# Kernel optimization log

Hardware: AMD Instinct MI355X
Metric: run time of the kernel (lower is better)

The kernel has to match this reference:

```python
import jax, jax.numpy as jnp
import numpy as np

B, S, E, H, FF = 8, 1024, 1024, 16, 4096
DK = E // H
EPS = 1.1920929e-07  # torch RMSNorm default eps = finfo(float32).eps


def _rmsnorm(x, g):
    return x * jax.lax.rsqrt(jnp.mean(x * x, axis=-1, keepdims=True) + EPS) * g


def _rope(q, k):
    # q, k: [B, H, S, DK]; standard rotate-half RoPE, theta=10000
    d = q.shape[-1]
    s = q.shape[-2]
    inv_freq = 1.0 / (10000.0 ** (jnp.arange(0, d, 2, dtype=jnp.float32) / d))
    ang = jnp.arange(s, dtype=jnp.float32)[:, None] * inv_freq  # [S, d/2]
    cos = jnp.concatenate([jnp.cos(ang), jnp.cos(ang)], axis=-1)  # [S, d]
    sin = jnp.concatenate([jnp.sin(ang), jnp.sin(ang)], axis=-1)

    def rot(x):
        x1, x2 = jnp.split(x, 2, axis=-1)
        return jnp.concatenate([-x2, x1], axis=-1)

    return q * cos + rot(q) * sin, k * cos + rot(k) * sin


def setup_inputs() -> dict:
    key = jax.random.key(0)
    ks = jax.random.split(key, 16)
    sc = 0.02
    inp = {
        "x": jax.random.normal(ks[0], (B, S, E), dtype=jnp.float32),
        "WQ": jax.random.normal(ks[1], (E, E), dtype=jnp.float32) * sc,
        "bQ": jnp.zeros((E,), jnp.float32),
        "WK": jax.random.normal(ks[2], (E, E), dtype=jnp.float32) * sc,
        "bK": jnp.zeros((E,), jnp.float32),
        "WV": jax.random.normal(ks[3], (E, E), dtype=jnp.float32) * sc,
        "bV": jnp.zeros((E,), jnp.float32),
        "WO": jax.random.normal(ks[4], (E, E), dtype=jnp.float32) * sc,
        "bO": jnp.zeros((E,), jnp.float32),
        "W1": jax.random.normal(ks[5], (E, FF), dtype=jnp.float32) * sc,
        "b1": jnp.zeros((FF,), jnp.float32),
        "W2": jax.random.normal(ks[6], (FF, E), dtype=jnp.float32) * sc,
        "b2": jnp.zeros((E,), jnp.float32),
        "g1": jnp.ones((E,), jnp.float32),
        "g2": jnp.ones((E,), jnp.float32),
    }
    return inp


def reference(x, WQ, bQ, WK, bK, WV, bV, WO, bO, W1, b1, W2, b2, g1, g2):
    b, s, e = x.shape

    def attn(h):
        q = (h @ WQ + bQ).reshape(b, s, H, DK).transpose(0, 2, 1, 3)
        k = (h @ WK + bK).reshape(b, s, H, DK).transpose(0, 2, 1, 3)
        v = (h @ WV + bV).reshape(b, s, H, DK).transpose(0, 2, 1, 3)
        q, k = _rope(q, k)
        scores = jnp.einsum("bhqd,bhkd->bhqk", q, k) / jnp.sqrt(jnp.float32(DK))
        p = jax.nn.softmax(scores, axis=-1)
        o = jnp.einsum("bhqk,bhkd->bhqd", p, v)
        o = o.transpose(0, 2, 1, 3).reshape(b, s, e)
        return o @ WO + bO

    def ffn(h):
        return jax.nn.relu(h @ W1 + b1) @ W2 + b2

    x = x + attn(_rmsnorm(x, g1))
    x = x + ffn(_rmsnorm(x, g2))
    return x
```

## Files before the change

### kernel.cpp

```cpp
#include <hip/hip_runtime.h>
#include <math.h>

#define B_ 8
#define S_ 1024
#define E_ 1024
#define H_ 16
#define FF_ 4096

typedef __attribute__((ext_vector_type(8))) short bf16x8;
typedef __attribute__((ext_vector_type(4))) float f32x4;

#define QSCALE 0.1803368801111f
#define LG2_10K 0.4152410118f

__device__ __forceinline__ unsigned short f2bf(float f) {
  union { float f; unsigned u; } v;
  v.f = f;
  unsigned r = v.u + 0x7fffu + ((v.u >> 16) & 1u);
  return (unsigned short)(r >> 16);
}
__device__ __forceinline__ float bf2f(unsigned short u) {
  union { unsigned u; float f; } v;
  v.u = ((unsigned)u) << 16;
  return v.f;
}
__device__ __forceinline__ unsigned fbits(float f) {
  union { float f; unsigned u; } v;
  v.f = f;
  return v.u;
}

__device__ __forceinline__ void glds16(const void* g, void* l) {
  __builtin_amdgcn_global_load_lds(
      (const __attribute__((address_space(1))) unsigned int*)g,
      (__attribute__((address_space(3))) unsigned int*)l, 16, 0, 0);
}

__global__ __launch_bounds__(256) void prep(const float* __restrict__ WQ,
                                            const float* __restrict__ WK,
                                            const float* __restrict__ WV,
                                            const float* __restrict__ WO,
                                            const float* __restrict__ W1,
                                            const float* __restrict__ W2,
                                            const float* __restrict__ bQ,
                                            const float* __restrict__ bK,
                                            const float* __restrict__ bV,
                                            unsigned short* __restrict__ WQKVt,
                                            unsigned short* __restrict__ WOt,
                                            unsigned short* __restrict__ W1t,
                                            unsigned short* __restrict__ W2t,
                                            float* __restrict__ bqkv) {
  const int id = blockIdx.x;
  if (id >= 12288) {
    const int i = (id - 12288) * 256 + threadIdx.x;
    if (i < 3072)
      bqkv[i] = (i < 1024) ? bQ[i] : ((i < 2048) ? bK[i - 1024] : bV[i - 2048]);
    return;
  }
  const float* W;
  unsigned short* D;
  int K, N, x, y;
  if (id < 4096) {
    const int m = id >> 10;
    const float* ws4[4] = {WQ, WK, WV, WO};
    unsigned short* ds4[4] = {WQKVt, WQKVt + 1024 * 1024, WQKVt + 2 * 1024 * 1024, WOt};
    W = ws4[m]; D = ds4[m]; K = 1024; N = 1024;
    x = id & 31; y = (id >> 5) & 31;
  } else if (id < 8192) {
    const int j = id - 4096;
    W = W1; D = W1t; K = 1024; N = 4096;
    x = j & 127; y = j >> 7;
  } else {
    const int j = id - 8192;
    W = W2; D = W2t; K = 4096; N = 1024;
    x = j & 31; y = j >> 5;
  }
  __shared__ float t[32][33];
  const int tx = threadIdx.x & 31, ty = threadIdx.x >> 5;
  const int n0 = x * 32, k0 = y * 32;
#pragma unroll
  for (int p = 0; p < 4; ++p)
    t[ty + p * 8][tx] = W[(size_t)(k0 + ty + p * 8) * N + n0 + tx];
  __syncthreads();
#pragma unroll
  for (int p = 0; p < 4; ++p)
    D[(size_t)(n0 + ty + p * 8) * K + k0 + tx] = f2bf(t[tx][ty + p * 8]);
}

__global__ __launch_bounds__(256) void rmsnorm_kernel(const float* __restrict__ x,
                                                      const float* __restrict__ g,
                                                      unsigned short* __restrict__ out) {
  const int row = blockIdx.x;
  const int t = threadIdx.x;
  const float4 v = ((const float4*)(x + (size_t)row * E_))[t];
  float ss = v.x * v.x + v.y * v.y + v.z * v.z + v.w * v.w;
#pragma unroll
  for (int off = 32; off > 0; off >>= 1) ss += __shfl_down(ss, off);
  __shared__ float sred[4];
  if ((t & 63) == 0) sred[t >> 6] = ss;
  __syncthreads();
  const float tot = sred[0] + sred[1] + sred[2] + sred[3];
  const float rinv = rsqrtf(tot * (1.0f / E_) + 1.1920929e-07f);
  const float4 gv = ((const float4*)g)[t];
  ushort4 o;
  o.x = f2bf(v.x * rinv * gv.x);
  o.y = f2bf(v.y * rinv * gv.y);
  o.z = f2bf(v.z * rinv * gv.z);
  o.w = f2bf(v.w * rinv * gv.w);
  ((ushort4*)(out + (size_t)row * E_))[t] = o;
}


template <int OUT_BF16, int RELU, int RES>
__global__ __launch_bounds__(256) void gemm_bf16(const unsigned short* __restrict__ A,
                                                 const unsigned short* __restrict__ Bt,
                                                 const float* __restrict__ bias,
                                                 const float* __restrict__ res,
                                                 void* __restrict__ C,
                                                 int M, int N, int K) {
  __shared__ unsigned short As[128 * 64];
  __shared__ unsigned short Bs[128 * 64];
  const int tid = threadIdx.x;
  const int w = tid >> 6;
  const int lane = tid & 63;

  const int nb = gridDim.x;
  const int id = blockIdx.x;
  const int lid = (id & 7) * (nb >> 3) + (id >> 3);
  const int per = (M >> 7) * 8;
  const int grp = lid / per;
  const int rem = lid - grp * per;
  const int bn = (grp * 8 + (rem & 7)) * 128;
  const int bm = (rem >> 3) * 128;

  const int wm = (w & 1) * 64, wn = (w >> 1) * 64;

  f32x4 acc[4][4];
#pragma unroll
  for (int i = 0; i < 4; ++i)
#pragma unroll
    for (int j = 0; j < 4; ++j) acc[i][j] = (f32x4){0.f, 0.f, 0.f, 0.f};

  const int srow = lane >> 3;
  const int skb = (lane & 7) ^ srow;
  const unsigned short* Ap[4];
  const unsigned short* Bp[4];
  unsigned short* AsD[4];
  unsigned short* BsD[4];
#pragma unroll
  for (int p = 0; p < 4; ++p) {
    const int u = w * 4 + p;
    Ap[p] = A + (size_t)(bm + u * 8 + srow) * K + skb * 8;
    Bp[p] = Bt + (size_t)(bn + u * 8 + srow) * K + skb * 8;
    AsD[p] = &As[u * 512 + lane * 8];
    BsD[p] = &Bs[u * 512 + lane * 8];
  }

  const int fr = lane & 15;
  const int g = lane >> 4;
  const int sw = fr & 7;

  for (int k0 = 0; k0 < K; k0 += 64) {
    __syncthreads();
#pragma unroll
    for (int p = 0; p < 4; ++p) glds16(Ap[p] + k0, AsD[p]);
#pragma unroll
    for (int p = 0; p < 4; ++p) glds16(Bp[p] + k0, BsD[p]);
    __syncthreads();
    bf16x8 a[4][2], b[4][2];
#pragma unroll
    for (int im = 0; im < 4; ++im)
#pragma unroll
      for (int kc = 0; kc < 2; ++kc)
        a[im][kc] = *(const bf16x8*)&As[(wm + im * 16 + fr) * 64 + ((kc * 4 + g) ^ sw) * 8];
#pragma unroll
    for (int in = 0; in < 4; ++in)
#pragma unroll
      for (int kc = 0; kc < 2; ++kc)
        b[in][kc] = *(const bf16x8*)&Bs[(wn + in * 16 + fr) * 64 + ((kc * 4 + g) ^ sw) * 8];
#pragma unroll
    for (int im = 0; im < 4; ++im)
#pragma unroll
      for (int in = 0; in < 4; ++in) {
        acc[im][in] = __builtin_amdgcn_mfma_f32_16x16x32_bf16(a[im][0], b[in][0], acc[im][in], 0, 0, 0);
        acc[im][in] = __builtin_amdgcn_mfma_f32_16x16x32_bf16(a[im][1], b[in][1], acc[im][in], 0, 0, 0);
      }
  }

#pragma unroll
  for (int im = 0; im < 4; ++im) {
    const int row0 = bm + wm + im * 16 + (lane >> 4) * 4;
#pragma unroll
    for (int in = 0; in < 4; ++in) {
      const int col = bn + wn + in * 16 + fr;
      const float bv = bias[col];
#pragma unroll
      for (int r = 0; r < 4; ++r) {
        float v = acc[im][in][r] + bv;
        if (RES) v += res[(size_t)(row0 + r) * N + col];
        if (RELU) v = fmaxf(v, 0.0f);
        if (OUT_BF16)
          ((unsigned short*)C)[(size_t)(row0 + r) * N + col] = f2bf(v);
        else
          ((float*)C)[(size_t)(row0 + r) * N + col] = v;
      }
    }
  }
}

__global__ __launch_bounds__(256) void gemm_sk2(const unsigned short* __restrict__ A,
                                                const unsigned short* __restrict__ Bt,
                                                unsigned short* __restrict__ Pp) {
  const int N = 1024, K = 4096, KH = 2048;
  __shared__ unsigned short As[128 * 64];
  __shared__ unsigned short Bs[128 * 64];
  const int tid = threadIdx.x;
  const int w = tid >> 6;
  const int lane = tid & 63;

  const int id = blockIdx.x;
  const int kh = id >> 9;
  const int hid = id & 511;
  const int lid = (hid & 7) * 64 + (hid >> 3);
  const int bn = (lid & 7) * 128;
  const int bm = (lid >> 3) * 128;

  const int wm = (w & 1) * 64, wn = (w >> 1) * 64;

  f32x4 acc[4][4];
#pragma unroll
  for (int i = 0; i < 4; ++i)
#pragma unroll
    for (int j = 0; j < 4; ++j) acc[i][j] = (f32x4){0.f, 0.f, 0.f, 0.f};

  const int srow = lane >> 3;
  const int skb = (lane & 7) ^ srow;
  const unsigned short* Ap[4];
  const unsigned short* Bp[4];
  unsigned short* AsD[4];
  unsigned short* BsD[4];
#pragma unroll
  for (int p = 0; p < 4; ++p) {
    const int u = w * 4 + p;
    Ap[p] = A + (size_t)(bm + u * 8 + srow) * K + kh * KH + skb * 8;
    Bp[p] = Bt + (size_t)(bn + u * 8 + srow) * K + kh * KH + skb * 8;
    AsD[p] = &As[u * 512 + lane * 8];
    BsD[p] = &Bs[u * 512 + lane * 8];
  }

  const int fr = lane & 15;
  const int g = lane >> 4;
  const int sw = fr & 7;

  for (int k0 = 0; k0 < KH; k0 += 64) {
    __syncthreads();
#pragma unroll
    for (int p = 0; p < 4; ++p) glds16(Ap[p] + k0, AsD[p]);
#pragma unroll
    for (int p = 0; p < 4; ++p) glds16(Bp[p] + k0, BsD[p]);
    __syncthreads();
    bf16x8 a[4][2], b[4][2];
#pragma unroll
    for (int im = 0; im < 4; ++im)
#pragma unroll
      for (int kc = 0; kc < 2; ++kc)
        a[im][kc] = *(const bf16x8*)&As[(wm + im * 16 + fr) * 64 + ((kc * 4 + g) ^ sw) * 8];
#pragma unroll
    for (int in = 0; in < 4; ++in)
#pragma unroll
      for (int kc = 0; kc < 2; ++kc)
        b[in][kc] = *(const bf16x8*)&Bs[(wn + in * 16 + fr) * 64 + ((kc * 4 + g) ^ sw) * 8];
#pragma unroll
    for (int im = 0; im < 4; ++im)
#pragma unroll
      for (int in = 0; in < 4; ++in) {
        acc[im][in] = __builtin_amdgcn_mfma_f32_16x16x32_bf16(a[im][0], b[in][0], acc[im][in], 0, 0, 0);
        acc[im][in] = __builtin_amdgcn_mfma_f32_16x16x32_bf16(a[im][1], b[in][1], acc[im][in], 0, 0, 0);
      }
  }

  unsigned short* P = Pp + (size_t)kh * (8u << 20);
#pragma unroll
  for (int im = 0; im < 4; ++im) {
    const int row0 = bm + wm + im * 16 + (lane >> 4) * 4;
#pragma unroll
    for (int in = 0; in < 4; ++in) {
      const int col = bn + wn + in * 16 + fr;
#pragma unroll
      for (int r = 0; r < 4; ++r)
        P[(size_t)(row0 + r) * N + col] = f2bf(acc[im][in][r]);
    }
  }
}

__global__ __launch_bounds__(256) void ff2_reduce(const unsigned short* __restrict__ Pp,
                                                  const float* __restrict__ x1,
                                                  const float* __restrict__ b2,
                                                  float* __restrict__ out) {
  const int i = blockIdx.x * 256 + threadIdx.x;
  const size_t off = (size_t)i * 4;
  const ushort4 p0 = *(const ushort4*)(Pp + off);
  const ushort4 p1 = *(const ushort4*)(Pp + (8u << 20) + off);
  const float4 xv = *(const float4*)(x1 + off);
  const float4 bv = *(const float4*)(b2 + (off & 1023));
  float4 o;
  o.x = xv.x + bv.x + bf2f(p0.x) + bf2f(p1.x);
  o.y = xv.y + bv.y + bf2f(p0.y) + bf2f(p1.y);
  o.z = xv.z + bv.z + bf2f(p0.z) + bf2f(p1.z);
  o.w = xv.w + bv.w + bf2f(p0.w) + bf2f(p1.w);
  *(float4*)(out + off) = o;
}

template <int OUT_BF16, int RELU, int RES>
__global__ __launch_bounds__(256) void gemm_n64(const unsigned short* __restrict__ A,
                                                const unsigned short* __restrict__ Bt,
                                                const float* __restrict__ bias,
                                                const float* __restrict__ res,
                                                void* __restrict__ C,
                                                int M, int N, int K) {
  __shared__ unsigned short As[128 * 64];
  __shared__ unsigned short Bs[64 * 64];
  const int tid = threadIdx.x;
  const int w = tid >> 6;
  const int lane = tid & 63;

  const int nbn = N >> 6;
  const int bm = (blockIdx.x / nbn) * 128;
  const int bn = (blockIdx.x % nbn) * 64;

  const int wm = (w & 1) * 64, wn = (w >> 1) * 32;

  f32x4 acc[4][2];
#pragma unroll
  for (int i = 0; i < 4; ++i)
#pragma unroll
    for (int j = 0; j < 2; ++j) acc[i][j] = (f32x4){0.f, 0.f, 0.f, 0.f};

  const int srow = lane >> 3;
  const int skb = (lane & 7) ^ srow;
  const unsigned short* Ap[4];
  const unsigned short* Bp[2];
  unsigned short* AsD[4];
  unsigned short* BsD[2];
#pragma unroll
  for (int p = 0; p < 4; ++p) {
    const int u = w * 4 + p;
    Ap[p] = A + (size_t)(bm + u * 8 + srow) * K + skb * 8;
    AsD[p] = &As[u * 512 + lane * 8];
  }
#pragma unroll
  for (int p = 0; p < 2; ++p) {
    const int u = w * 2 + p;
    Bp[p] = Bt + (size_t)(bn + u * 8 + srow) * K + skb * 8;
    BsD[p] = &Bs[u * 512 + lane * 8];
  }

  const int fr = lane & 15;
  const int g = lane >> 4;
  const int sw = fr & 7;

  for (int k0 = 0; k0 < K; k0 += 64) {
    __syncthreads();
#pragma unroll
    for (int p = 0; p < 4; ++p) glds16(Ap[p] + k0, AsD[p]);
#pragma unroll
    for (int p = 0; p < 2; ++p) glds16(Bp[p] + k0, BsD[p]);
    __syncthreads();
    bf16x8 a[4][2], b[2][2];
#pragma unroll
    for (int im = 0; im < 4; ++im)
#pragma unroll
      for (int kc = 0; kc < 2; ++kc)
        a[im][kc] = *(const bf16x8*)&As[(wm + im * 16 + fr) * 64 + ((kc * 4 + g) ^ sw) * 8];
#pragma unroll
    for (int in = 0; in < 2; ++in)
#pragma unroll
      for (int kc = 0; kc < 2; ++kc)
        b[in][kc] = *(const bf16x8*)&Bs[(wn + in * 16 + fr) * 64 + ((kc * 4 + g) ^ sw) * 8];
#pragma unroll
    for (int im = 0; im < 4; ++im)
#pragma unroll
      for (int in = 0; in < 2; ++in) {
        acc[im][in] = __builtin_amdgcn_mfma_f32_16x16x32_bf16(a[im][0], b[in][0], acc[im][in], 0, 0, 0);
        acc[im][in] = __builtin_amdgcn_mfma_f32_16x16x32_bf16(a[im][1], b[in][1], acc[im][in], 0, 0, 0);
      }
  }

#pragma unroll
  for (int im = 0; im < 4; ++im) {
    const int row0 = bm + wm + im * 16 + (lane >> 4) * 4;
#pragma unroll
    for (int in = 0; in < 2; ++in) {
      const int col = bn + wn + in * 16 + fr;
      const float bv = bias[col];
#pragma unroll
      for (int r = 0; r < 4; ++r) {
        float v = acc[im][in][r] + bv;
        if (RES) v += res[(size_t)(row0 + r) * N + col];
        if (RELU) v = fmaxf(v, 0.0f);
        if (OUT_BF16)
          ((unsigned short*)C)[(size_t)(row0 + r) * N + col] = f2bf(v);
        else
          ((float*)C)[(size_t)(row0 + r) * N + col] = v;
      }
    }
  }
}

__global__ __launch_bounds__(256) void gemm_qkv(const unsigned short* __restrict__ A,
                                                const unsigned short* __restrict__ Bt,
                                                const float* __restrict__ bias,
                                                unsigned short* __restrict__ QKV,
                                                unsigned short* __restrict__ Vt,
                                                int M, int K) {
  __shared__ unsigned short As[128 * 64];
  __shared__ unsigned short Bs[128 * 64];
  const int tid = threadIdx.x;
  const int w = tid >> 6;
  const int lane = tid & 63;

  const int nb = gridDim.x;
  const int id = blockIdx.x;
  const int lid = (id & 7) * (nb >> 3) + (id >> 3);
  const int per = (M >> 7) * 8;
  const int grp = lid / per;
  const int rem = lid - grp * per;
  const int bn = (grp * 8 + (rem & 7)) * 128;
  const int bm = (rem >> 3) * 128;

  const int wm = (w & 1) * 64, wn = (w >> 1) * 64;

  f32x4 acc[4][4];
#pragma unroll
  for (int i = 0; i < 4; ++i)
#pragma unroll
    for (int j = 0; j < 4; ++j) acc[i][j] = (f32x4){0.f, 0.f, 0.f, 0.f};

  const int srow = lane >> 3;
  const int skb = (lane & 7) ^ srow;
  const unsigned short* Ap[4];
  const unsigned short* Bp[4];
  unsigned short* AsD[4];
  unsigned short* BsD[4];
#pragma unroll
  for (int p = 0; p < 4; ++p) {
    const int u = w * 4 + p;
    Ap[p] = A + (size_t)(bm + u * 8 + srow) * K + skb * 8;
    Bp[p] = Bt + (size_t)(bn + u * 8 + srow) * K + skb * 8;
    AsD[p] = &As[u * 512 + lane * 8];
    BsD[p] = &Bs[u * 512 + lane * 8];
  }

  const int fr = lane & 15;
  const int g = lane >> 4;
  const int sw = fr & 7;

  for (int k0 = 0; k0 < K; k0 += 64) {
    __syncthreads();
#pragma unroll
    for (int p = 0; p < 4; ++p) glds16(Ap[p] + k0, AsD[p]);
#pragma unroll
    for (int p = 0; p < 4; ++p) glds16(Bp[p] + k0, BsD[p]);
    __syncthreads();
    bf16x8 a[4][2], b[4][2];
#pragma unroll
    for (int im = 0; im < 4; ++im)
#pragma unroll
      for (int kc = 0; kc < 2; ++kc)
        a[im][kc] = *(const bf16x8*)&As[(wm + im * 16 + fr) * 64 + ((kc * 4 + g) ^ sw) * 8];
#pragma unroll
    for (int in = 0; in < 4; ++in)
#pragma unroll
      for (int kc = 0; kc < 2; ++kc)
        b[in][kc] = *(const bf16x8*)&Bs[(wn + in * 16 + fr) * 64 + ((kc * 4 + g) ^ sw) * 8];
#pragma unroll
    for (int im = 0; im < 4; ++im)
#pragma unroll
      for (int in = 0; in < 4; ++in) {
        acc[im][in] = __builtin_amdgcn_mfma_f32_16x16x32_bf16(a[im][0], b[in][0], acc[im][in], 0, 0, 0);
        acc[im][in] = __builtin_amdgcn_mfma_f32_16x16x32_bf16(a[im][1], b[in][1], acc[im][in], 0, 0, 0);
      }
  }

  const int cbase = bn + wn;
  const int seg = cbase >> 6;
  const int typ = seg >> 4;
  const int hh = seg & 15;
  const int bidx = bm >> 10;
  float bv[4];
#pragma unroll
  for (int in = 0; in < 4; ++in) bv[in] = bias[cbase + in * 16 + fr];

  if (typ == 2) {
#pragma unroll
    for (int im = 0; im < 4; ++im) {
      const int s0 = (bm & 1023) + wm + im * 16 + (lane >> 4) * 4;
#pragma unroll
      for (int in = 0; in < 4; ++in) {
        const int d = in * 16 + fr;
        ushort4 o4;
        o4.x = f2bf(acc[im][in][0] + bv[in]);
        o4.y = f2bf(acc[im][in][1] + bv[in]);
        o4.z = f2bf(acc[im][in][2] + bv[in]);
        o4.w = f2bf(acc[im][in][3] + bv[in]);
        *(ushort4*)&Vt[(size_t)((bidx * 16 + hh) * 64 + d) * S_ + s0] = o4;
      }
    }
  } else {
    const float qs = (typ == 0) ? QSCALE : 1.0f;
    const float i0 = exp2f(-LG2_10K * (float)fr);
    const float i1 = exp2f(-LG2_10K * (float)(fr + 16));
#pragma unroll
    for (int im = 0; im < 4; ++im) {
      const int row0 = bm + wm + im * 16 + (lane >> 4) * 4;
#pragma unroll
      for (int r = 0; r < 4; ++r) {
        const int row = row0 + r;
        const float s = (float)(row & 1023);
        float sn0, cs0, sn1, cs1;
        __sincosf(s * i0, &sn0, &cs0);
        __sincosf(s * i1, &sn1, &cs1);
        const float x0 = acc[im][0][r] + bv[0];
        const float x1 = acc[im][1][r] + bv[1];
        const float x2 = acc[im][2][r] + bv[2];
        const float x3 = acc[im][3][r] + bv[3];
        unsigned short* cp = QKV + (size_t)row * 3072 + cbase;
        cp[fr]      = f2bf((x0 * cs0 - x2 * sn0) * qs);
        cp[16 + fr] = f2bf((x1 * cs1 - x3 * sn1) * qs);
        cp[32 + fr] = f2bf((x2 * cs0 + x0 * sn0) * qs);
        cp[48 + fr] = f2bf((x3 * cs1 + x1 * sn1) * qs);
      }
    }
  }
}

__global__ __launch_bounds__(256) void attn_v4(const unsigned short* __restrict__ QKV,
                                               const unsigned short* __restrict__ Vt,
                                               unsigned short* __restrict__ Og) {
  __shared__ unsigned short Kf[2][8 * 512];
  __shared__ unsigned short Vf[2][8 * 512];
  __shared__ unsigned short Ps[4][32 * 72];
  const int tid = threadIdx.x;
  const int w = tid >> 6, lane = tid & 63;
  const int qt = blockIdx.x, bh = blockIdx.y;
  const int b = bh >> 4, h = bh & 15;
  const int fr = lane & 15, g = lane >> 4, fk = g * 8;
  const int q0w = qt * 128 + w * 32;

  bf16x8 qB[2][2];
#pragma unroll
  for (int nt = 0; nt < 2; ++nt)
#pragma unroll
    for (int c = 0; c < 2; ++c)
      qB[nt][c] = *(const bf16x8*)&QKV[(size_t)(b * S_ + q0w + nt * 16 + fr) * 3072 +
                                       h * 64 + c * 32 + fk];

  f32x4 o[4][2];
#pragma unroll
  for (int mt = 0; mt < 4; ++mt)
#pragma unroll
    for (int nt = 0; nt < 2; ++nt) o[mt][nt] = (f32x4){0.f, 0.f, 0.f, 0.f};
  float l[2] = {0.0f, 0.0f};

#define STAGE(kt, bufi)                                                                   \
  {                                                                                       \
    _Pragma("unroll") for (int p = 0; p < 4; ++p) {                                       \
      const int u = w * 4 + p;                                                            \
      if (u < 8) {                                                                        \
        const int mt = u >> 1, c = u & 1;                                                 \
        glds16(QKV + (size_t)(b * S_ + (kt) * 64 + mt * 16 + fr) * 3072 + 1024 + h * 64 + \
                   c * 32 + fk,                                                           \
               &Kf[bufi][u * 512]);                                                       \
      } else {                                                                            \
        const int v2 = u - 8, mt = v2 >> 1, c = v2 & 1;                                   \
        glds16(Vt + (size_t)(bh * 64 + mt * 16 + fr) * S_ + (kt) * 64 + c * 32 + fk,      \
               &Vf[bufi][v2 * 512]);                                                      \
      }                                                                                   \
    }                                                                                     \
  }

  STAGE(0, 0);

  for (int kt = 0; kt < 16; ++kt) {
    __syncthreads();
    if (kt < 15) STAGE(kt + 1, (kt + 1) & 1);
    const unsigned short* Kc = Kf[kt & 1];
    const unsigned short* Vc = Vf[kt & 1];

    f32x4 s[4][2];
#pragma unroll
    for (int mt = 0; mt < 4; ++mt) {
      const bf16x8 k0 = *(const bf16x8*)&Kc[(mt * 2 + 0) * 512 + lane * 8];
      const bf16x8 k1 = *(const bf16x8*)&Kc[(mt * 2 + 1) * 512 + lane * 8];
#pragma unroll
      for (int nt = 0; nt < 2; ++nt) {
        f32x4 a = (f32x4){0.f, 0.f, 0.f, 0.f};
        a = __builtin_amdgcn_mfma_f32_16x16x32_bf16(k0, qB[nt][0], a, 0, 0, 0);
        a = __builtin_amdgcn_mfma_f32_16x16x32_bf16(k1, qB[nt][1], a, 0, 0, 0);
        s[mt][nt] = a;
      }
    }

#pragma unroll
    for (int nt = 0; nt < 2; ++nt) {
      float rs = 0.0f;
#pragma unroll
      for (int mt = 0; mt < 4; ++mt)
#pragma unroll
        for (int r = 0; r < 4; ++r) {
          const float p = exp2f(s[mt][nt][r]);
          s[mt][nt][r] = p;
          rs += p;
        }
      rs += __shfl_xor(rs, 16);
      rs += __shfl_xor(rs, 32);
      l[nt] += rs;
    }

#pragma unroll
    for (int nt = 0; nt < 2; ++nt)
#pragma unroll
      for (int mt = 0; mt < 4; ++mt) {
        uint2 pk;
        pk.x = __builtin_amdgcn_perm(fbits(s[mt][nt][1]), fbits(s[mt][nt][0]), 0x07060302u);
        pk.y = __builtin_amdgcn_perm(fbits(s[mt][nt][3]), fbits(s[mt][nt][2]), 0x07060302u);
        *(uint2*)&Ps[w][(nt * 16 + fr) * 72 + mt * 16 + g * 4] = pk;
      }

    bf16x8 pB[2][2];
#pragma unroll
    for (int nt = 0; nt < 2; ++nt)
#pragma unroll
      for (int c = 0; c < 2; ++c)
        pB[nt][c] = *(const bf16x8*)&Ps[w][(nt * 16 + fr) * 72 + c * 32 + fk];
#pragma unroll
    for (int mt = 0; mt < 4; ++mt) {
      const bf16x8 v0 = *(const bf16x8*)&Vc[(mt * 2 + 0) * 512 + lane * 8];
      const bf16x8 v1 = *(const bf16x8*)&Vc[(mt * 2 + 1) * 512 + lane * 8];
#pragma unroll
      for (int nt = 0; nt < 2; ++nt) {
        o[mt][nt] = __builtin_amdgcn_mfma_f32_16x16x32_bf16(v0, pB[nt][0], o[mt][nt], 0, 0, 0);
        o[mt][nt] = __builtin_amdgcn_mfma_f32_16x16x32_bf16(v1, pB[nt][1], o[mt][nt], 0, 0, 0);
      }
    }
  }

  const float linv0 = 1.0f / l[0], linv1 = 1.0f / l[1];
#pragma unroll
  for (int nt = 0; nt < 2; ++nt) {
    const float li = nt ? linv1 : linv0;
#pragma unroll
    for (int mt = 0; mt < 4; ++mt) {
      uint2 pk;
      pk.x = __builtin_amdgcn_perm(fbits(o[mt][nt][1] * li), fbits(o[mt][nt][0] * li), 0x07060302u);
      pk.y = __builtin_amdgcn_perm(fbits(o[mt][nt][3] * li), fbits(o[mt][nt][2] * li), 0x07060302u);
      *(uint2*)&Ps[w][(nt * 16 + fr) * 72 + mt * 16 + g * 4] = pk;
    }
  }
  const int qr = lane >> 1, hf = lane & 1;
#pragma unroll
  for (int c = 0; c < 2; ++c) {
    const bf16x8 vv = *(const bf16x8*)&Ps[w][qr * 72 + hf * 16 + c * 32];
    *(bf16x8*)&Og[(size_t)(b * S_ + q0w + qr) * E_ + h * 64 + hf * 16 + c * 32] = vv;
  }
}

extern "C" void kernel_launch(void* const* d_in, const int* in_sizes, int n_in,
                              void* d_out, int out_size, void* d_ws, size_t ws_size,
                              hipStream_t stream) {
  const float* x  = (const float*)d_in[0];
  const float* WQ = (const float*)d_in[1];
  const float* bQ = (const float*)d_in[2];
  const float* WK = (const float*)d_in[3];
  const float* bK = (const float*)d_in[4];
  const float* WV = (const float*)d_in[5];
  const float* bV = (const float*)d_in[6];
  const float* WO = (const float*)d_in[7];
  const float* bO = (const float*)d_in[8];
  const float* W1 = (const float*)d_in[9];
  const float* b1 = (const float*)d_in[10];
  const float* W2 = (const float*)d_in[11];
  const float* b2 = (const float*)d_in[12];
  const float* g1 = (const float*)d_in[13];
  const float* g2 = (const float*)d_in[14];
  float* out = (float*)d_out;

  char* ws = (char*)d_ws;
  const size_t MB = 1024 * 1024;
  unsigned short* h1   = (unsigned short*)(ws + 0 * MB);
  unsigned short* QKV  = (unsigned short*)(ws + 16 * MB);
  unsigned short* Vt   = (unsigned short*)(ws + 64 * MB);
  unsigned short* Ob   = (unsigned short*)(ws + 80 * MB);
  float*          x1   = (float*)(ws + 96 * MB);
  unsigned short* h2   = (unsigned short*)(ws + 128 * MB);
  unsigned short* mid  = (unsigned short*)(ws + 16 * MB);
  unsigned short* WQKVt= (unsigned short*)(ws + 144 * MB);
  unsigned short* WOt  = (unsigned short*)(ws + 150 * MB);
  unsigned short* W1t  = (unsigned short*)(ws + 152 * MB);
  unsigned short* W2t  = (unsigned short*)(ws + 160 * MB);
  float*          bqkv = (float*)(ws + 168 * MB);
  unsigned short* Pp   = (unsigned short*)(ws + 176 * MB);

  const int M = B_ * S_;

  prep<<<12300, 256, 0, stream>>>(WQ, WK, WV, WO, W1, W2, bQ, bK, bV,
                                  WQKVt, WOt, W1t, W2t, bqkv);

  rmsnorm_kernel<<<M, 256, 0, stream>>>(x, g1, h1);

  gemm_qkv<<<24 * 64, 256, 0, stream>>>(h1, WQKVt, bqkv, QKV, Vt, M, E_);

  attn_v4<<<dim3(8, B_ * H_), 256, 0, stream>>>(QKV, Vt, Ob);

  gemm_n64<0, 0, 1><<<64 * 16, 256, 0, stream>>>(Ob, WOt, bO, x, x1, M, E_, E_);

  rmsnorm_kernel<<<M, 256, 0, stream>>>(x1, g2, h2);

  gemm_bf16<1, 1, 0><<<32 * 64, 256, 0, stream>>>(h2, W1t, b1, nullptr, mid, M, FF_, E_);

  gemm_sk2<<<1024, 256, 0, stream>>>(mid, W2t, Pp);

  ff2_reduce<<<8192, 256, 0, stream>>>(Pp, x1, b2, out);
}
```

Before: 493.1 us.

## Replace FFN GEMMs with 256x256-tile double-buffered 512-thread GEMM kernel

Replaces the 128x128-tile FFN GEMMs (W1 with ReLU, and the split-K W2) with one templated kernel. It uses 256x256 tiles, 8 waves, and double-buffered LDS with async global-to-LDS loads gated by vmcnt waits, plus setprio around the MFMA blocks. Larger tiles raise operand reuse per LDS load, and prefetching two stages ahead overlaps memory with MFMA. In exchange it uses 128KB of LDS and many more accumulator registers per thread, and launches fewer blocks (512 and 256), which may hurt occupancy and tail balance.

```diff
diff --git a/kernel.cpp b/kernel.cpp
--- a/kernel.cpp
+++ b/kernel.cpp
@@ -110,34 +110,35 @@
   ((ushort4*)(out + (size_t)row * E_))[t] = o;
 }
 
-
-template <int OUT_BF16, int RELU, int RES>
-__global__ __launch_bounds__(256) void gemm_bf16(const unsigned short* __restrict__ A,
-                                                 const unsigned short* __restrict__ Bt,
-                                                 const float* __restrict__ bias,
-                                                 const float* __restrict__ res,
-                                                 void* __restrict__ C,
-                                                 int M, int N, int K) {
-  __shared__ unsigned short As[128 * 64];
-  __shared__ unsigned short Bs[128 * 64];
+template <int EPI, int SPLIT>
+__global__ __launch_bounds__(512, 2) void gemm256(const unsigned short* __restrict__ A,
+                                                  const unsigned short* __restrict__ Bt,
+                                                  const float* __restrict__ bias,
+                                                  unsigned short* __restrict__ C,
+                                                  int M, int N, int K) {
+  __shared__ unsigned short Ls[2][2][256 * 64];
   const int tid = threadIdx.x;
   const int w = tid >> 6;
   const int lane = tid & 63;
 
-  const int nb = gridDim.x;
-  const int id = blockIdx.x;
+  int id = blockIdx.x;
+  int kh = 0;
+  int nb = gridDim.x;
+  if (SPLIT) { kh = id >> 7; id &= 127; nb = 128; }
   const int lid = (id & 7) * (nb >> 3) + (id >> 3);
-  const int per = (M >> 7) * 8;
-  const int grp = lid / per;
-  const int rem = lid - grp * per;
-  const int bn = (grp * 8 + (rem & 7)) * 128;
-  const int bm = (rem >> 3) * 128;
-
-  const int wm = (w & 1) * 64, wn = (w >> 1) * 64;
-
-  f32x4 acc[4][4];
-#pragma unroll
-  for (int i = 0; i < 4; ++i)
+  const int nbn = N >> 8;
+  const int bm = (lid / nbn) * 256;
+  const int bn = (lid % nbn) * 256;
+
+  const int Kloc = SPLIT ? (K >> 1) : K;
+  const unsigned short* Ab = A + (size_t)kh * Kloc;
+  const unsigned short* Bb = Bt + (size_t)kh * Kloc;
+
+  const int wm = (w & 1) * 128, wn = (w >> 1) * 64;
+
+  f32x4 acc[8][4];
+#pragma unroll
+  for (int i = 0; i < 8; ++i)
 #pragma unroll
     for (int j = 0; j < 4; ++j) acc[i][j] = (f32x4){0.f, 0.f, 0.f, 0.f};
 
@@ -145,152 +146,97 @@
   const int skb = (lane & 7) ^ srow;
   const unsigned short* Ap[4];
   const unsigned short* Bp[4];
-  unsigned short* AsD[4];
-  unsigned short* BsD[4];
 #pragma unroll
   for (int p = 0; p < 4; ++p) {
     const int u = w * 4 + p;
-    Ap[p] = A + (size_t)(bm + u * 8 + srow) * K + skb * 8;
-    Bp[p] = Bt + (size_t)(bn + u * 8 + srow) * K + skb * 8;
-    AsD[p] = &As[u * 512 + lane * 8];
-    BsD[p] = &Bs[u * 512 + lane * 8];
+    Ap[p] = Ab + (size_t)(bm + u * 8 + srow) * K + skb * 8;
+    Bp[p] = Bb + (size_t)(bn + u * 8 + srow) * K + skb * 8;
   }
 
   const int fr = lane & 15;
   const int g = lane >> 4;
   const int sw = fr & 7;
 
-  for (int k0 = 0; k0 < K; k0 += 64) {
-    __syncthreads();
-#pragma unroll
-    for (int p = 0; p < 4; ++p) glds16(Ap[p] + k0, AsD[p]);
-#pragma unroll
-    for (int p = 0; p < 4; ++p) glds16(Bp[p] + k0, BsD[p]);
-    __syncthreads();
-    bf16x8 a[4][2], b[4][2];
-#pragma unroll
-    for (int im = 0; im < 4; ++im)
-#pragma unroll
-      for (int kc = 0; kc < 2; ++kc)
-        a[im][kc] = *(const bf16x8*)&As[(wm + im * 16 + fr) * 64 + ((kc * 4 + g) ^ sw) * 8];
-#pragma unroll
-    for (int in = 0; in < 4; ++in)
-#pragma unroll
-      for (int kc = 0; kc < 2; ++kc)
-        b[in][kc] = *(const bf16x8*)&Bs[(wn + in * 16 + fr) * 64 + ((kc * 4 + g) ^ sw) * 8];
-#pragma unroll
-    for (int im = 0; im < 4; ++im)
+#define ISSUE256(tt, bi)                                              \
+  {                                                                   \
+    _Pragma("unroll") for (int p = 0; p < 4; ++p) {                   \
+      const int u = w * 4 + p;                                        \
+      glds16(Ap[p] + (size_t)(tt) * 64, &Ls[bi][0][u * 512 + lane * 8]); \
+    }                                                                 \
+    _Pragma("unroll") for (int p = 0; p < 4; ++p) {                   \
+      const int u = w * 4 + p;                                        \
+      glds16(Bp[p] + (size_t)(tt) * 64, &Ls[bi][1][u * 512 + lane * 8]); \
+    }                                                                 \
+  }
+
+  const int nt = Kloc >> 6;
+  ISSUE256(0, 0);
+  ISSUE256(1, 1);
+
+  for (int t = 0; t < nt; ++t) {
+    if (t < nt - 1)
+      asm volatile("s_waitcnt vmcnt(8)" ::: "memory");
+    else
+      asm volatile("s_waitcnt vmcnt(0)" ::: "memory");
+    __builtin_amdgcn_s_barrier();
+    __builtin_amdgcn_sched_barrier(0);
+
+    const unsigned short* Ac = &Ls[t & 1][0][0];
+    const unsigned short* Bc = &Ls[t & 1][1][0];
+#pragma unroll
+    for (int kc = 0; kc < 2; ++kc) {
+      bf16x8 a[8], b[4];
+#pragma unroll
+      for (int im = 0; im < 8; ++im)
+        a[im] = *(const bf16x8*)&Ac[(wm + im * 16 + fr) * 64 + (((kc * 4 + g) ^ sw)) * 8];
+#pragma unroll
+      for (int in = 0; in < 4; ++in)
+        b[in] = *(const bf16x8*)&Bc[(wn + in * 16 + fr) * 64 + (((kc * 4 + g) ^ sw)) * 8];
+      __builtin_amdgcn_s_setprio(1);
+#pragma unroll
+      for (int im = 0; im < 8; ++im)
+#pragma unroll
+        for (int in = 0; in < 4; ++in)
+          acc[im][in] = __builtin_amdgcn_mfma_f32_16x16x32_bf16(a[im], b[in], acc[im][in], 0, 0, 0);
+      __builtin_amdgcn_s_setprio(0);
+    }
+
+    __builtin_amdgcn_sched_barrier(0);
+    __builtin_amdgcn_s_barrier();
+    if (t + 2 < nt) ISSUE256(t + 2, t & 1);
+  }
+
+  if (EPI == 0) {
+#pragma unroll
+    for (int im = 0; im < 8; ++im) {
+      const int row0 = bm + wm + im * 16 + g * 4;
 #pragma unroll
       for (int in = 0; in < 4; ++in) {
-        acc[im][in] = __builtin_amdgcn_mfma_f32_16x16x32_bf16(a[im][0], b[in][0], acc[im][in], 0, 0, 0);
-        acc[im][in] = __builtin_amdgcn_mfma_f32_16x16x32_bf16(a[im][1], b[in][1], acc[im][in], 0, 0, 0);
-      }
-  }
-
-#pragma unroll
-  for (int im = 0; im < 4; ++im) {
-    const int row0 = bm + wm + im * 16 + (lane >> 4) * 4;
-#pragma unroll
-    for (int in = 0; in < 4; ++in) {
-      const int col = bn + wn + in * 16 + fr;
-      const float bv = bias[col];
-#pragma unroll
-      for (int r = 0; r < 4; ++r) {
-        float v = acc[im][in][r] + bv;
-        if (RES) v += res[(size_t)(row0 + r) * N + col];
-        if (RELU) v = fmaxf(v, 0.0f);
-        if (OUT_BF16)
-          ((unsigned short*)C)[(size_t)(row0 + r) * N + col] = f2bf(v);
-        else
-          ((float*)C)[(size_t)(row0 + r) * N + col] = v;
-      }
-    }
-  }
-}
-
-__global__ __launch_bounds__(256) void gemm_sk2(const unsigned short* __restrict__ A,
-                                                const unsigned short* __restrict__ Bt,
-                                                unsigned short* __restrict__ Pp) {
-  const int N = 1024, K = 4096, KH = 2048;
-  __shared__ unsigned short As[128 * 64];
-  __shared__ unsigned short Bs[128 * 64];
-  const int tid = threadIdx.x;
-  const int w = tid >> 6;
-  const int lane = tid & 63;
-
-  const int id = blockIdx.x;
-  const int kh = id >> 9;
-  const int hid = id & 511;
-  const int lid = (hid & 7) * 64 + (hid >> 3);
-  const int bn = (lid & 7) * 128;
-  const int bm = (lid >> 3) * 128;
-
-  const int wm = (w & 1) * 64, wn = (w >> 1) * 64;
-
-  f32x4 acc[4][4];
-#pragma unroll
-  for (int i = 0; i < 4; ++i)
-#pragma unroll
-    for (int j = 0; j < 4; ++j) acc[i][j] = (f32x4){0.f, 0.f, 0.f, 0.f};
-
-  const int srow = lane >> 3;
-  const int skb = (lane & 7) ^ srow;
-  const unsigned short* Ap[4];
-  const unsigned short* Bp[4];
-  unsigned short* AsD[4];
-  unsigned short* BsD[4];
-#pragma unroll
-  for (int p = 0; p < 4; ++p) {
-    const int u = w * 4 + p;
-    Ap[p] = A + (size_t)(bm + u * 8 + srow) * K + kh * KH + skb * 8;
-    Bp[p] = Bt + (size_t)(bn + u * 8 + srow) * K + kh * KH + skb * 8;
-    AsD[p] = &As[u * 512 + lane * 8];
-    BsD[p] = &Bs[u * 512 + lane * 8];
-  }
-
-  const int fr = lane & 15;
-  const int g = lane >> 4;
-  const int sw = fr & 7;
-
-  for (int k0 = 0; k0 < KH; k0 += 64) {
-    __syncthreads();
-#pragma unroll
-    for (int p = 0; p < 4; ++p) glds16(Ap[p] + k0, AsD[p]);
-#pragma unroll
-    for (int p = 0; p < 4; ++p) glds16(Bp[p] + k0, BsD[p]);
-    __syncthreads();
-    bf16x8 a[4][2], b[4][2];
-#pragma unroll
-    for (int im = 0; im < 4; ++im)
-#pragma unroll
-      for (int kc = 0; kc < 2; ++kc)
-        a[im][kc] = *(const bf16x8*)&As[(wm + im * 16 + fr) * 64 + ((kc * 4 + g) ^ sw) * 8];
-#pragma unroll
-    for (int in = 0; in < 4; ++in)
-#pragma unroll
-      for (int kc = 0; kc < 2; ++kc)
-        b[in][kc] = *(const bf16x8*)&Bs[(wn + in * 16 + fr) * 64 + ((kc * 4 + g) ^ sw) * 8];
-#pragma unroll
-    for (int im = 0; im < 4; ++im)
+        const int col = bn + wn + in * 16 + fr;
+        const float bv = bias[col];
+#pragma unroll
+        for (int r = 0; r < 4; ++r) {
+          float v = acc[im][in][r] + bv;
+          v = fmaxf(v, 0.0f);
+          C[(size_t)(row0 + r) * N + col] = f2bf(v);
+        }
+      }
+    }
+  } else {
+    unsigned short* P = C + (size_t)kh * ((size_t)M * N);
+#pragma unroll
+    for (int im = 0; im < 8; ++im) {
+      const int row0 = bm + wm + im * 16 + g * 4;
 #pragma unroll
       for (int in = 0; in < 4; ++in) {
-        acc[im][in] = __builtin_amdgcn_mfma_f32_16x16x32_bf16(a[im][0], b[in][0], acc[im][in], 0, 0, 0);
-        acc[im][in] = __builtin_amdgcn_mfma_f32_16x16x32_bf16(a[im][1], b[in][1], acc[im][in], 0, 0, 0);
-      }
-  }
-
-  unsigned short* P = Pp + (size_t)kh * (8u << 20);
-#pragma unroll
-  for (int im = 0; im < 4; ++im) {
-    const int row0 = bm + wm + im * 16 + (lane >> 4) * 4;
-#pragma unroll
-    for (int in = 0; in < 4; ++in) {
-      const int col = bn + wn + in * 16 + fr;
-#pragma unroll
-      for (int r = 0; r < 4; ++r)
-        P[(size_t)(row0 + r) * N + col] = f2bf(acc[im][in][r]);
-    }
-  }
+        const int col = bn + wn + in * 16 + fr;
+#pragma unroll
+        for (int r = 0; r < 4; ++r)
+          P[(size_t)(row0 + r) * N + col] = f2bf(acc[im][in][r]);
+      }
+    }
+  }
+#undef ISSUE256
 }
 
 __global__ __launch_bounds__(256) void ff2_reduce(const unsigned short* __restrict__ Pp,
@@ -716,9 +662,9 @@
 
   rmsnorm_kernel<<<M, 256, 0, stream>>>(x1, g2, h2);
 
-  gemm_bf16<1, 1, 0><<<32 * 64, 256, 0, stream>>>(h2, W1t, b1, nullptr, mid, M, FF_, E_);
-
-  gemm_sk2<<<1024, 256, 0, stream>>>(mid, W2t, Pp);
+  gemm256<0, 0><<<512, 512, 0, stream>>>(h2, W1t, b1, mid, M, FF_, E_);
+
+  gemm256<1, 1><<<256, 512, 0, stream>>>(mid, W2t, nullptr, Pp, M, 1024, 4096);
 
   ff2_reduce<<<8192, 256, 0, stream>>>(Pp, x1, b2, out);
 }
```

After: 479.4 us. 1.03x faster.
